# Performance work log

Hardware: AMD Instinct MI355X
Metric: run time of the kernel (lower is better)

## Reference

```python
import jax, jax.numpy as jnp
import numpy as np

D = 128        # embed_dims
P = 4          # num_points
G = 1          # num_groups
L = 4          # num_levels
NC = 6         # cameras
HB, WB = 200, 200
QN = HB * WB
NUM_LAYERS = 2
IMG_H, IMG_W = 256, 704
EPS = 1e-5
PC_MIN = np.array([-50.0, -50.0, -5.0], np.float32)
PC_EXT = np.array([100.0, 100.0, 8.0], np.float32)
LEVEL_HW = [(32, 88), (16, 44), (8, 22), (4, 11)]


def layer_norm(x, g, b):
    m = x.mean(-1, keepdims=True)
    v = jnp.mean((x - m) ** 2, axis=-1, keepdims=True)
    return (x - m) * jax.lax.rsqrt(v + 1e-5) * g + b


def bilinear(feat, u, v):
    # feat: (B,H,W,C); u,v: (B,N) normalized to [0,1]; zero padding, align_corners=False
    B, H, W, C = feat.shape
    x = u * W - 0.5
    y = v * H - 0.5
    x0f = jnp.floor(x)
    y0f = jnp.floor(y)
    wx = (x - x0f)[..., None]
    wy = (y - y0f)[..., None]
    x0 = x0f.astype(jnp.int32)
    y0 = y0f.astype(jnp.int32)
    bi = jnp.arange(B)[:, None]

    def gather(xi, yi):
        valid = ((xi >= 0) & (xi < W) & (yi >= 0) & (yi < H)).astype(feat.dtype)[..., None]
        return feat[bi, jnp.clip(yi, 0, H - 1), jnp.clip(xi, 0, W - 1)] * valid

    return (gather(x0, y0) * (1 - wx) * (1 - wy)
            + gather(x0 + 1, y0) * wx * (1 - wy)
            + gather(x0, y0 + 1) * (1 - wx) * wy
            + gather(x0 + 1, y0 + 1) * wx * wy)


def cam_contrib(l2i_n, hom, sw, cam_feats):
    # l2i_n: (B,4,4); hom: (B,Q,G,P,4); sw: (B,Q,G,P,L); cam_feats: L x (B,Hl,Wl,C)
    p2 = jnp.einsum('bij,bqgpj->bqgpi', l2i_n, hom)
    z = p2[..., 2]
    zc = jnp.maximum(z, EPS)
    u = p2[..., 0] / (zc * IMG_W)
    v = p2[..., 1] / (zc * IMG_H)
    mask = (z > EPS) & (u >= 0) & (u <= 1) & (v >= 0) & (v <= 1)
    B = hom.shape[0]
    uf = u.reshape(B, -1)
    vf = v.reshape(B, -1)
    out = jnp.zeros(hom.shape[:4] + (cam_feats[0].shape[-1],), cam_feats[0].dtype)
    for l in range(L):
        s = bilinear(cam_feats[l], uf, vf).reshape(B, -1, G, P, cam_feats[l].shape[-1])
        out = out + s * sw[..., l:l + 1]
    return out * mask[..., None].astype(out.dtype)


def forward(feat0, feat1, feat2, feat3, lidar2img, bev_query, bev_pos,
            pe_w1, pe_b1, pe_w2, pe_b2, conv1_w, conv1_b, conv2_w, conv2_b,
            off_w, off_b, sw_w, sw_b, cp_w1, cp_b1, cp_w2, cp_b2, cp_w3, cp_b3,
            ffn_w1, ffn_b1, ffn_w2, ffn_b2, n1_g, n1_b, n2_g, n2_b, n3_g, n3_b):
    # (b,n,C,h,w) -> (b,n,h,w,C), matching the decoder's rearrange (g=1)
    feats = [jnp.transpose(f, (0, 1, 3, 4, 2)) for f in (feat0, feat1, feat2, feat3)]
    B = bev_query.shape[0]
    pc_min = jnp.asarray(PC_MIN)
    pc_ext = jnp.asarray(PC_EXT)
    # position embedding of bev_pos is identical every layer
    pos_embed = jax.nn.relu(bev_pos @ pe_w1 + pe_b1) @ pe_w2 + pe_b2
    q = bev_query
    for _ in range(NUM_LAYERS):
        # in_conv: 1x1 conv + GELU + 5x5 conv on 200x200 BEV grid
        qe = (q + pos_embed).reshape(B, HB, WB, D)
        h = jax.nn.gelu(qe @ conv1_w + conv1_b, approximate=False)
        h = jax.lax.conv_general_dilated(h, conv2_w, (1, 1), 'SAME',
                                         dimension_numbers=('NHWC', 'HWIO', 'NHWC')) + conv2_b
        q = q + h.reshape(B, QN, D)
        q = layer_norm(q, n1_g, n1_b)
        # DetSegSampling
        off = (q @ off_w + off_b).reshape(B, QN, G, P, 3)
        ref = bev_pos[:, :, None, None, :] * pc_ext + pc_min
        pts = ref + off
        sw = jax.nn.softmax((q @ sw_w + sw_b).reshape(B, QN, G, P, L), axis=-1)
        hom = jnp.concatenate([pts, jnp.ones_like(pts[..., :1])], -1)
        acc = jnp.zeros((B, QN, G, P, D), q.dtype)
        for n in range(NC):
            acc = acc + cam_contrib(lidar2img[:, n], hom, sw,
                                    tuple(f[:, n] for f in feats))
        # 'b q g p c -> b q (p g c)' then 3-layer compressor MLP (1x1 convs)
        flat = jnp.transpose(acc, (0, 1, 3, 2, 4)).reshape(B, QN, P * G * D)
        h = jax.nn.relu(flat @ cp_w1 + cp_b1)
        h = jax.nn.relu(h @ cp_w2 + cp_b2)
        h = h @ cp_w3 + cp_b3
        q = q + h
        q = layer_norm(q, n2_g, n2_b)
        q = q + (jax.nn.relu(q @ ffn_w1 + ffn_b1) @ ffn_w2 + ffn_b2)
        q = layer_norm(q, n3_g, n3_b)
    return q


def _make_lidar2img():
    fx = fy = 500.0
    K = np.array([[fx, 0, IMG_W / 2, 0], [0, fy, IMG_H / 2, 0],
                  [0, 0, 1, 0], [0, 0, 0, 1]], np.float32)
    mats = []
    for n in range(NC):
        yaw = 2 * np.pi * n / NC
        c, s = np.cos(yaw), np.sin(yaw)
        # camera n looks along (cos yaw, sin yaw, 0), mounted 1.5m above lidar
        E = np.array([[s, -c, 0, 0], [0, 0, -1, 1.5], [c, s, 0, 0], [0, 0, 0, 1]], np.float32)
        mats.append(K @ E)
    return jnp.asarray(np.stack(mats))[None]  # (1,NC,4,4)


def setup_inputs() -> dict:
    key = jax.random.key(0)
    ks = jax.random.split(key, 24)
    sc = 0.02
    inp = {}
    for i, (h, w) in enumerate(LEVEL_HW):
        inp[f'feat{i}'] = jax.random.normal(ks[i], (1, NC, D, h, w), jnp.float32)
    inp['lidar2img'] = _make_lidar2img()
    inp['bev_query'] = jax.random.normal(ks[4], (1, QN, D), jnp.float32)
    inp['bev_pos'] = jax.random.uniform(ks[5], (1, QN, 3), jnp.float32)
    inp['pe_w1'] = jax.random.normal(ks[6], (3, 2 * D), jnp.float32) * sc
    inp['pe_b1'] = jnp.zeros((2 * D,), jnp.float32)
    inp['pe_w2'] = jax.random.normal(ks[7], (2 * D, D), jnp.float32) * sc
    inp['pe_b2'] = jnp.zeros((D,), jnp.float32)
    inp['conv1_w'] = jax.random.normal(ks[8], (D, D), jnp.float32) * sc
    inp['conv1_b'] = jnp.zeros((D,), jnp.float32)
    inp['conv2_w'] = jax.random.normal(ks[9], (5, 5, D, D), jnp.float32) * sc
    inp['conv2_b'] = jnp.zeros((D,), jnp.float32)
    inp['off_w'] = jax.random.normal(ks[10], (D, G * P * 3), jnp.float32) * 0.01
    inp['off_b'] = jax.random.uniform(ks[11], (G * P * 3,), jnp.float32, -0.5, 0.5)
    inp['sw_w'] = jax.random.normal(ks[12], (D, G * P * L), jnp.float32) * sc
    inp['sw_b'] = jnp.zeros((G * P * L,), jnp.float32)
    inp['cp_w1'] = jax.random.normal(ks[13], (P * G * D, 4 * D), jnp.float32) * sc
    inp['cp_b1'] = jnp.zeros((4 * D,), jnp.float32)
    inp['cp_w2'] = jax.random.normal(ks[14], (4 * D, 4 * D), jnp.float32) * sc
    inp['cp_b2'] = jnp.zeros((4 * D,), jnp.float32)
    inp['cp_w3'] = jax.random.normal(ks[15], (4 * D, D), jnp.float32) * sc
    inp['cp_b3'] = jnp.zeros((D,), jnp.float32)
    inp['ffn_w1'] = jax.random.normal(ks[16], (D, D), jnp.float32) * sc
    inp['ffn_b1'] = jnp.zeros((D,), jnp.float32)
    inp['ffn_w2'] = jax.random.normal(ks[17], (D, D), jnp.float32) * sc
    inp['ffn_b2'] = jnp.zeros((D,), jnp.float32)
    for i in (1, 2, 3):
        inp[f'n{i}_g'] = jnp.ones((D,), jnp.float32)
        inp[f'n{i}_b'] = jnp.zeros((D,), jnp.float32)
    return inp


def reference(feat0, feat1, feat2, feat3, lidar2img, bev_query, bev_pos,
              pe_w1, pe_b1, pe_w2, pe_b2, conv1_w, conv1_b, conv2_w, conv2_b,
              off_w, off_b, sw_w, sw_b, cp_w1, cp_b1, cp_w2, cp_b2, cp_w3, cp_b3,
              ffn_w1, ffn_b1, ffn_w2, ffn_b2, n1_g, n1_b, n2_g, n2_b, n3_g, n3_b):
    return forward(feat0, feat1, feat2, feat3, lidar2img, bev_query, bev_pos,
                   pe_w1, pe_b1, pe_w2, pe_b2, conv1_w, conv1_b, conv2_w, conv2_b,
                   off_w, off_b, sw_w, sw_b, cp_w1, cp_b1, cp_w2, cp_b2, cp_w3, cp_b3,
                   ffn_w1, ffn_b1, ffn_w2, ffn_b2, n1_g, n1_b, n2_g, n2_b, n3_g, n3_b)
```

## Files before the change

kernel.cpp:

```cpp
#include <hip/hip_runtime.h>
#include <hip/hip_bf16.h>

typedef unsigned short u16;
typedef unsigned char u8;
typedef __attribute__((ext_vector_type(8))) short bf16x8;
typedef __attribute__((ext_vector_type(4))) float f32x4;

#define DEV __device__ __forceinline__

DEV float b2f(u16 s){ return __uint_as_float(((unsigned)s) << 16); }
DEV u16 f2b(float f){
    unsigned u = __float_as_uint(f);
    u = u + 0x7fffu + ((u >> 16) & 1u);
    return (u16)(u >> 16);
}
DEV u8 f2f8(float v){
    int r = __builtin_amdgcn_cvt_pk_fp8_f32(v, v, 0, false);
    return (u8)(r & 0xff);
}
DEV unsigned f2f8x4(float a, float b, float c, float d){
    int lo = __builtin_amdgcn_cvt_pk_fp8_f32(a, b, 0, false);
    int r  = __builtin_amdgcn_cvt_pk_fp8_f32(c, d, lo, true);
    return (unsigned)r;
}
DEV void storeElem(float* p, float v){ *p = v; }
DEV void storeElem(u16* p, float v){ *p = f2b(v); }
DEV void storeElem(u8* p, float v){ *p = f2f8(v); }

template<int ACT> DEV float actf(float x){
    if (ACT == 1) return fmaxf(x, 0.f);
    if (ACT == 2) return 0.5f * x * (1.f + erff(x * 0.70710678118654752f));
    return x;
}

DEV void gload16(const void* g, void* l){
    __builtin_amdgcn_global_load_lds(
        (const __attribute__((address_space(1))) void*)g,
        (__attribute__((address_space(3))) void*)l, 16, 0, 0);
}

__global__ void transpose_feat(const float* __restrict__ in, u16* __restrict__ out,
                               int H, int W){
    int total = 6 * H * W * 32;
    int lin = blockIdx.x * 256 + threadIdx.x;
    if (lin >= total) return;
    int c4   = (lin & 31) * 4;
    int pix  = lin >> 5;
    int x    = pix % W;
    int rest = pix / W;
    int y    = rest % H;
    int n    = rest / H;
    int HW   = H * W;
    size_t ib = ((size_t)(n * 128 + c4) * H + y) * W + x;
    ushort4 v;
    v.x = f2b(in[ib]);
    v.y = f2b(in[ib + (size_t)HW]);
    v.z = f2b(in[ib + (size_t)2 * HW]);
    v.w = f2b(in[ib + (size_t)3 * HW]);
    *(ushort4*)&out[(size_t)pix * 128 + c4] = v;
}

__global__ void prep_wt(const float* __restrict__ w, u16* __restrict__ o, int K, int N){
    int id = blockIdx.x * 256 + threadIdx.x;
    if (id >= K * N) return;
    int n = id / K, k = id % K;
    o[id] = f2b(w[(size_t)k * N + n]);
}
__global__ void prep_wt_f8(const float* __restrict__ w, u8* __restrict__ o, int K, int N){
    int id = blockIdx.x * 256 + threadIdx.x;
    if (id >= K * N) return;
    int n = id / K, k = id % K;
    o[id] = f2f8(w[(size_t)k * N + n]);
}
__global__ void prep_osw_w(const float* __restrict__ off_w, const float* __restrict__ off_b,
                           const float* __restrict__ sw_w, const float* __restrict__ sw_b,
                           u16* __restrict__ owsT, float* __restrict__ obias){
    int id = blockIdx.x * 256 + threadIdx.x;
    if (id >= 4096) return;
    int n = id >> 7, k = id & 127;
    float w = (n < 12) ? off_w[k * 12 + n] : (n < 28) ? sw_w[k * 16 + (n - 12)] : 0.f;
    owsT[n * 128 + k] = f2b(w);
    if (k == 0) obias[n] = (n < 12) ? off_b[n] : (n < 28) ? sw_b[n - 12] : 0.f;
}
__global__ void prep_conv_w_f8(const float* __restrict__ w, u8* __restrict__ o){
    int id = blockIdx.x * 256 + threadIdx.x;
    if (id >= 51200) return;
    int slot = id & 15;
    int oc   = (id >> 4) & 127;
    int tap  = id >> 11;
    int ks = slot >> 2, kg = slot & 3;
    int ic0 = ks * 32 + kg * 8;
    u8 tmp[8];
#pragma unroll
    for (int j = 0; j < 8; j++)
        tmp[j] = f2f8(w[((size_t)tap * 128 + ic0 + j) * 128 + oc]);
    *(long*)&o[(size_t)tap * 16384 + ks * 4096 + kg * 1024 + oc * 8] = *(long*)tmp;
}
__global__ void prep_hid(const float* __restrict__ bev_pos,
                         const float* __restrict__ w1, const float* __restrict__ b1,
                         u16* __restrict__ hid){
    int id = blockIdx.x * 256 + threadIdx.x;
    if (id >= 2560000) return;
    int qi = id >> 6, c4 = (id & 63) * 4;
    float p0 = bev_pos[qi * 3 + 0];
    float p1 = bev_pos[qi * 3 + 1];
    float p2 = bev_pos[qi * 3 + 2];
    ushort4 v;
    u16* vp = (u16*)&v;
#pragma unroll
    for (int j = 0; j < 4; j++){
        int ch = c4 + j;
        float h = p0 * w1[ch] + p1 * w1[256 + ch] + p2 * w1[512 + ch] + b1[ch];
        vp[j] = f2b(fmaxf(h, 0.f));
    }
    *(ushort4*)&hid[(size_t)qi * 256 + c4] = v;
}

DEV void stage64(const u16* __restrict__ g, int ldk, u16* lds, int wv, int lane){
    const u16* gp = g + (size_t)(lane >> 3) * ldk + (lane & 7) * 8;
#pragma unroll
    for (int j = 0; j < 4; j++){
        int ch = wv + j * 4;
        gload16(gp + (size_t)ch * 8 * ldk, lds + ch * 512);
    }
}
DEV void stage64f8(const u8* __restrict__ g, int ldk, u8* lds, int wv, int lane){
    int rloc = lane >> 2;
#pragma unroll
    for (int j = 0; j < 2; j++){
        int ch = wv + j * 4;
        int row = ch * 16 + rloc;
        int sp  = (lane & 3) ^ ((row >> 1) & 3);
        gload16(g + (size_t)row * ldk + sp * 16, lds + ch * 1024);
    }
}

template<int K, int ACT, typename TOUT, int NBY = 0, int NBX = 0>
__global__ __launch_bounds__(256) void mfma_gemm(
    const u16* __restrict__ A, const u16* __restrict__ BT,
    const float* __restrict__ bias, TOUT* __restrict__ C, int Ntot){
    __shared__ u16 As[2][128 * 64];
    __shared__ u16 Bs[2][128 * 64];
    const int t = threadIdx.x, wv = t >> 6, lane = t & 63;
    int bx, by;
    if (NBY > 0){
        const int gpx = (NBX + 7) / 8;
        int xcd = blockIdx.x & 7, slot = blockIdx.x >> 3;
        bx = xcd * gpx + slot / NBY;
        by = slot % NBY;
        if (bx >= NBX) return;
    } else { bx = blockIdx.x; by = blockIdx.y; }
    const int r0 = bx * 128, n0 = by * 128;
    const int l15 = lane & 15, kg = lane >> 4;
    const int wr = (wv >> 1) * 64, wc = (wv & 1) * 64;
    f32x4 acc[4][4];
#pragma unroll
    for (int r = 0; r < 4; r++)
#pragma unroll
        for (int c = 0; c < 4; c++) acc[r][c] = (f32x4){0.f, 0.f, 0.f, 0.f};

    stage64(A + (size_t)r0 * K, K, As[0], wv, lane);
    stage64(BT + (size_t)n0 * K, K, Bs[0], wv, lane);
    __syncthreads();
    int buf = 0;
    for (int kc = 0; kc < K / 64; kc++){
        if (kc + 1 < K / 64){
            stage64(A + (size_t)r0 * K + (kc + 1) * 64, K, As[buf ^ 1], wv, lane);
            stage64(BT + (size_t)n0 * K + (kc + 1) * 64, K, Bs[buf ^ 1], wv, lane);
        }
#pragma unroll
        for (int ks = 0; ks < 2; ks++){
            bf16x8 af[4], bfr[4];
#pragma unroll
            for (int r = 0; r < 4; r++)
                af[r] = *(const bf16x8*)&As[buf][(wr + r * 16 + l15) * 64 + ks * 32 + kg * 8];
#pragma unroll
            for (int c = 0; c < 4; c++)
                bfr[c] = *(const bf16x8*)&Bs[buf][(wc + c * 16 + l15) * 64 + ks * 32 + kg * 8];
#pragma unroll
            for (int r = 0; r < 4; r++)
#pragma unroll
                for (int c = 0; c < 4; c++)
                    acc[r][c] = __builtin_amdgcn_mfma_f32_16x16x32_bf16(af[r], bfr[c], acc[r][c], 0, 0, 0);
        }
        __syncthreads();
        buf ^= 1;
    }
#pragma unroll
    for (int c = 0; c < 4; c++){
        int gcol = n0 + wc + c * 16 + l15;
        float bb = bias[gcol];
#pragma unroll
        for (int r = 0; r < 4; r++){
#pragma unroll
            for (int reg = 0; reg < 4; reg++){
                int grow = r0 + wr + r * 16 + kg * 4 + reg;
                storeElem(C + (size_t)grow * Ntot + gcol, actf<ACT>(acc[r][c][reg] + bb));
            }
        }
    }
}

template<int K, int ACT, typename TOUT, int NBY = 0, int NBX = 0>
__global__ __launch_bounds__(256) void mfma_gemm_f8(
    const u8* __restrict__ A, const u8* __restrict__ BT,
    const float* __restrict__ bias, TOUT* __restrict__ C, int Ntot){
    __shared__ __align__(16) u8 As[2][128 * 64];
    __shared__ __align__(16) u8 Bs[2][128 * 64];
    const int t = threadIdx.x, wv = t >> 6, lane = t & 63;
    int bx, by;
    if (NBY > 0){
        const int gpx = (NBX + 7) / 8;
        int xcd = blockIdx.x & 7, slot = blockIdx.x >> 3;
        bx = xcd * gpx + slot / NBY;
        by = slot % NBY;
        if (bx >= NBX) return;
    } else { bx = blockIdx.x; by = blockIdx.y; }
    const int r0 = bx * 128, n0 = by * 128;
    const int l15 = lane & 15, kg = lane >> 4;
    const int wr = (wv >> 1) * 64, wc = (wv & 1) * 64;
    f32x4 acc[4][4];
#pragma unroll
    for (int r = 0; r < 4; r++)
#pragma unroll
        for (int c = 0; c < 4; c++) acc[r][c] = (f32x4){0.f, 0.f, 0.f, 0.f};

    stage64f8(A + (size_t)r0 * K, K, As[0], wv, lane);
    stage64f8(BT + (size_t)n0 * K, K, Bs[0], wv, lane);
    __syncthreads();
    int buf = 0;
    for (int kc = 0; kc < K / 64; kc++){
        if (kc + 1 < K / 64){
            stage64f8(A + (size_t)r0 * K + (kc + 1) * 64, K, As[buf ^ 1], wv, lane);
            stage64f8(BT + (size_t)n0 * K + (kc + 1) * 64, K, Bs[buf ^ 1], wv, lane);
        }
#pragma unroll
        for (int ks = 0; ks < 2; ks++){
            long af[4], bfr[4];
#pragma unroll
            for (int r = 0; r < 4; r++){
                int row = wr + r * 16 + l15;
                int s8 = (ks * 4 + kg) ^ (row & 6);
                af[r] = *(const long*)&As[buf][row * 64 + s8 * 8];
            }
#pragma unroll
            for (int c = 0; c < 4; c++){
                int row = wc + c * 16 + l15;
                int s8 = (ks * 4 + kg) ^ (row & 6);
                bfr[c] = *(const long*)&Bs[buf][row * 64 + s8 * 8];
            }
#pragma unroll
            for (int r = 0; r < 4; r++)
#pragma unroll
                for (int c = 0; c < 4; c++)
                    acc[r][c] = __builtin_amdgcn_mfma_f32_16x16x32_fp8_fp8(af[r], bfr[c], acc[r][c], 0, 0, 0);
        }
        __syncthreads();
        buf ^= 1;
    }
#pragma unroll
    for (int c = 0; c < 4; c++){
        int gcol = n0 + wc + c * 16 + l15;
        float bb = bias[gcol];
#pragma unroll
        for (int r = 0; r < 4; r++){
#pragma unroll
            for (int reg = 0; reg < 4; reg++){
                int grow = r0 + wr + r * 16 + kg * 4 + reg;
                storeElem(C + (size_t)grow * Ntot + gcol, actf<ACT>(acc[r][c][reg] + bb));
            }
        }
    }
}

__global__ __launch_bounds__(256) void mfma_pos(
    const u16* __restrict__ A, const u16* __restrict__ BT,
    const float* __restrict__ bias, const float* __restrict__ bq,
    float* __restrict__ pos, u16* __restrict__ qp16){
    const int K = 256;
    __shared__ u16 As[2][128 * 64];
    __shared__ u16 Bs[2][128 * 64];
    const int t = threadIdx.x, wv = t >> 6, lane = t & 63;
    const int r0 = blockIdx.x * 128;
    const int l15 = lane & 15, kg = lane >> 4;
    const int wr = (wv >> 1) * 64, wc = (wv & 1) * 64;
    f32x4 acc[4][4];
#pragma unroll
    for (int r = 0; r < 4; r++)
#pragma unroll
        for (int c = 0; c < 4; c++) acc[r][c] = (f32x4){0.f, 0.f, 0.f, 0.f};

    stage64(A + (size_t)r0 * K, K, As[0], wv, lane);
    stage64(BT, K, Bs[0], wv, lane);
    __syncthreads();
    int buf = 0;
    for (int kc = 0; kc < 4; kc++){
        if (kc + 1 < 4){
            stage64(A + (size_t)r0 * K + (kc + 1) * 64, K, As[buf ^ 1], wv, lane);
            stage64(BT + (kc + 1) * 64, K, Bs[buf ^ 1], wv, lane);
        }
#pragma unroll
        for (int ks = 0; ks < 2; ks++){
            bf16x8 af[4], bfr[4];
#pragma unroll
            for (int r = 0; r < 4; r++)
                af[r] = *(const bf16x8*)&As[buf][(wr + r * 16 + l15) * 64 + ks * 32 + kg * 8];
#pragma unroll
            for (int c = 0; c < 4; c++)
                bfr[c] = *(const bf16x8*)&Bs[buf][(wc + c * 16 + l15) * 64 + ks * 32 + kg * 8];
#pragma unroll
            for (int r = 0; r < 4; r++)
#pragma unroll
                for (int c = 0; c < 4; c++)
                    acc[r][c] = __builtin_amdgcn_mfma_f32_16x16x32_bf16(af[r], bfr[c], acc[r][c], 0, 0, 0);
        }
        __syncthreads();
        buf ^= 1;
    }
#pragma unroll
    for (int c = 0; c < 4; c++){
        int gcol = wc + c * 16 + l15;
        float bb = bias[gcol];
#pragma unroll
        for (int r = 0; r < 4; r++){
#pragma unroll
            for (int reg = 0; reg < 4; reg++){
                int grow = r0 + wr + r * 16 + kg * 4 + reg;
                int growc = min(grow, 39999);
                float v = acc[r][c][reg] + bb;
                pos[(size_t)grow * 128 + gcol]  = v;
                qp16[(size_t)grow * 128 + gcol] = f2b(v + bq[(size_t)growc * 128 + gcol]);
            }
        }
    }
}

template<int K, int AUXM>
__global__ __launch_bounds__(256) void mfma_gemm_ln(
    const u16* __restrict__ A, const u16* __restrict__ BT,
    const float* __restrict__ bias, const float* __restrict__ qin,
    const float* __restrict__ gam, const float* __restrict__ bet,
    float* __restrict__ outf, u16* __restrict__ aux,
    const float* __restrict__ pos, int Mlim){
    __shared__ u16 As[2][128 * 64];
    __shared__ u16 Bs[2][128 * 64];
    const int t = threadIdx.x, wv = t >> 6, lane = t & 63;
    const int r0 = blockIdx.x * 128;
    const int l15 = lane & 15, kg = lane >> 4;
    const int wr = wv * 32;
    f32x4 acc[2][8];
#pragma unroll
    for (int r = 0; r < 2; r++)
#pragma unroll
        for (int c = 0; c < 8; c++) acc[r][c] = (f32x4){0.f, 0.f, 0.f, 0.f};

    stage64(A + (size_t)r0 * K, K, As[0], wv, lane);
    stage64(BT, K, Bs[0], wv, lane);
    __syncthreads();
    int buf = 0;
    for (int kc = 0; kc < K / 64; kc++){
        if (kc + 1 < K / 64){
            stage64(A + (size_t)r0 * K + (kc + 1) * 64, K, As[buf ^ 1], wv, lane);
            stage64(BT + (kc + 1) * 64, K, Bs[buf ^ 1], wv, lane);
        }
#pragma unroll
        for (int ks = 0; ks < 2; ks++){
            bf16x8 af[2], bfr[8];
#pragma unroll
            for (int r = 0; r < 2; r++)
                af[r] = *(const bf16x8*)&As[buf][(wr + r * 16 + l15) * 64 + ks * 32 + kg * 8];
#pragma unroll
            for (int c = 0; c < 8; c++)
                bfr[c] = *(const bf16x8*)&Bs[buf][(c * 16 + l15) * 64 + ks * 32 + kg * 8];
#pragma unroll
            for (int r = 0; r < 2; r++)
#pragma unroll
                for (int c = 0; c < 8; c++)
                    acc[r][c] = __builtin_amdgcn_mfma_f32_16x16x32_bf16(af[r], bfr[c], acc[r][c], 0, 0, 0);
        }
        __syncthreads();
        buf ^= 1;
    }
    float bb[8], gg[8], be[8];
#pragma unroll
    for (int c = 0; c < 8; c++){
        int col = c * 16 + l15;
        bb[c] = bias[col]; gg[c] = gam[col]; be[c] = bet[col];
    }
#pragma unroll
    for (int r = 0; r < 2; r++){
#pragma unroll
        for (int reg = 0; reg < 4; reg++){
            int grow = r0 + wr + r * 16 + kg * 4 + reg;
            const float* qrow = qin + (size_t)grow * 128;
            float s = 0.f, q2 = 0.f;
#pragma unroll
            for (int c = 0; c < 8; c++){
                float x = acc[r][c][reg] + bb[c] + qrow[c * 16 + l15];
                acc[r][c][reg] = x;
                s += x; q2 += x * x;
            }
#pragma unroll
            for (int m = 8; m >= 1; m >>= 1){
                s  += __shfl_xor(s, m, 64);
                q2 += __shfl_xor(q2, m, 64);
            }
            float mean = s * 0.0078125f;
            float var  = q2 * 0.0078125f - mean * mean;
            float rs   = rsqrtf(var + 1e-5f);
            bool wr_ok = grow < Mlim;
#pragma unroll
            for (int c = 0; c < 8; c++){
                float o = (acc[r][c][reg] - mean) * rs * gg[c] + be[c];
                int col = c * 16 + l15;
                if (wr_ok){
                    outf[(size_t)grow * 128 + col] = o;
                    if (AUXM == 1) aux[(size_t)grow * 128 + col] = f2b(o);
                    else if (AUXM == 2)
                        aux[(size_t)grow * 128 + col] = f2b(o + pos[(size_t)grow * 128 + col]);
                }
            }
        }
    }
}

template<int K, int AUXM>
__global__ __launch_bounds__(256) void mfma_gemm_ln_f8(
    const u8* __restrict__ A, const u8* __restrict__ BT,
    const float* __restrict__ bias, const float* __restrict__ qin,
    const float* __restrict__ gam, const float* __restrict__ bet,
    float* __restrict__ outf, u16* __restrict__ aux,
    const float* __restrict__ pos, int Mlim){
    __shared__ __align__(16) u8 As[2][128 * 64];
    __shared__ __align__(16) u8 Bs[2][128 * 64];
    const int t = threadIdx.x, wv = t >> 6, lane = t & 63;
    const int r0 = blockIdx.x * 128;
    const int l15 = lane & 15, kg = lane >> 4;
    const int wr = wv * 32;
    f32x4 acc[2][8];
#pragma unroll
    for (int r = 0; r < 2; r++)
#pragma unroll
        for (int c = 0; c < 8; c++) acc[r][c] = (f32x4){0.f, 0.f, 0.f, 0.f};

    stage64f8(A + (size_t)r0 * K, K, As[0], wv, lane);
    stage64f8(BT, K, Bs[0], wv, lane);
    __syncthreads();
    int buf = 0;
    for (int kc = 0; kc < K / 64; kc++){
        if (kc + 1 < K / 64){
            stage64f8(A + (size_t)r0 * K + (kc + 1) * 64, K, As[buf ^ 1], wv, lane);
            stage64f8(BT + (kc + 1) * 64, K, Bs[buf ^ 1], wv, lane);
        }
#pragma unroll
        for (int ks = 0; ks < 2; ks++){
            long af[2], bfr[8];
#pragma unroll
            for (int r = 0; r < 2; r++){
                int row = wr + r * 16 + l15;
                int s8 = (ks * 4 + kg) ^ (row & 6);
                af[r] = *(const long*)&As[buf][row * 64 + s8 * 8];
            }
#pragma unroll
            for (int c = 0; c < 8; c++){
                int row = c * 16 + l15;
                int s8 = (ks * 4 + kg) ^ (row & 6);
                bfr[c] = *(const long*)&Bs[buf][row * 64 + s8 * 8];
            }
#pragma unroll
            for (int r = 0; r < 2; r++)
#pragma unroll
                for (int c = 0; c < 8; c++)
                    acc[r][c] = __builtin_amdgcn_mfma_f32_16x16x32_fp8_fp8(af[r], bfr[c], acc[r][c], 0, 0, 0);
        }
        __syncthreads();
        buf ^= 1;
    }
    float bb[8], gg[8], be[8];
#pragma unroll
    for (int c = 0; c < 8; c++){
        int col = c * 16 + l15;
        bb[c] = bias[col]; gg[c] = gam[col]; be[c] = bet[col];
    }
#pragma unroll
    for (int r = 0; r < 2; r++){
#pragma unroll
        for (int reg = 0; reg < 4; reg++){
            int grow = r0 + wr + r * 16 + kg * 4 + reg;
            const float* qrow = qin + (size_t)grow * 128;
            float s = 0.f, q2 = 0.f;
#pragma unroll
            for (int c = 0; c < 8; c++){
                float x = acc[r][c][reg] + bb[c] + qrow[c * 16 + l15];
                acc[r][c][reg] = x;
                s += x; q2 += x * x;
            }
#pragma unroll
            for (int m = 8; m >= 1; m >>= 1){
                s  += __shfl_xor(s, m, 64);
                q2 += __shfl_xor(q2, m, 64);
            }
            float mean = s * 0.0078125f;
            float var  = q2 * 0.0078125f - mean * mean;
            float rs   = rsqrtf(var + 1e-5f);
            bool wr_ok = grow < Mlim;
#pragma unroll
            for (int c = 0; c < 8; c++){
                float o = (acc[r][c][reg] - mean) * rs * gg[c] + be[c];
                int col = c * 16 + l15;
                if (wr_ok){
                    outf[(size_t)grow * 128 + col] = o;
                    if (AUXM == 1) aux[(size_t)grow * 128 + col] = f2b(o);
                    else if (AUXM == 2)
                        aux[(size_t)grow * 128 + col] = f2b(o + pos[(size_t)grow * 128 + col]);
                }
            }
        }
    }
}

__global__ __launch_bounds__(256) void mfma_osw(
    const u16* __restrict__ A, const u16* __restrict__ BT,
    const float* __restrict__ bias, float* __restrict__ osw){
    __shared__ u16 As[2][128 * 64];
    __shared__ u16 Bs[2][32 * 64];
    const int t = threadIdx.x, wv = t >> 6, lane = t & 63;
    const int r0 = blockIdx.x * 128;
    const int l15 = lane & 15, kg = lane >> 4;
#pragma unroll
    for (int it = 0; it < 8; it++){
        int id = it * 256 + t;
        int row = id >> 4, slot = id & 15;
        uint4 v = *(const uint4*)&A[(size_t)(r0 + row) * 128 + slot * 8];
        *(uint4*)&As[slot >> 3][row * 64 + (slot & 7) * 8] = v;
    }
#pragma unroll
    for (int it = 0; it < 2; it++){
        int id = it * 256 + t;
        if (id < 512){
            int row = id >> 4, slot = id & 15;
            uint4 v = *(const uint4*)&BT[(size_t)row * 128 + slot * 8];
            *(uint4*)&Bs[slot >> 3][row * 64 + (slot & 7) * 8] = v;
        }
    }
    __syncthreads();
    f32x4 acc[2][2];
#pragma unroll
    for (int r = 0; r < 2; r++)
#pragma unroll
        for (int c = 0; c < 2; c++) acc[r][c] = (f32x4){0.f, 0.f, 0.f, 0.f};
#pragma unroll
    for (int ks = 0; ks < 4; ks++){
        int h = ks >> 1, koff = (ks & 1) * 32 + kg * 8;
        bf16x8 af[2], bfr[2];
#pragma unroll
        for (int r = 0; r < 2; r++)
            af[r] = *(const bf16x8*)&As[h][(wv * 32 + r * 16 + l15) * 64 + koff];
#pragma unroll
        for (int c = 0; c < 2; c++)
            bfr[c] = *(const bf16x8*)&Bs[h][(c * 16 + l15) * 64 + koff];
#pragma unroll
        for (int r = 0; r < 2; r++)
#pragma unroll
            for (int c = 0; c < 2; c++)
                acc[r][c] = __builtin_amdgcn_mfma_f32_16x16x32_bf16(af[r], bfr[c], acc[r][c], 0, 0, 0);
    }
#pragma unroll
    for (int c = 0; c < 2; c++){
        int gcol = c * 16 + l15;
        float bb = bias[gcol];
#pragma unroll
        for (int r = 0; r < 2; r++)
#pragma unroll
            for (int reg = 0; reg < 4; reg++){
                int grow = r0 + wv * 32 + r * 16 + kg * 4 + reg;
                osw[(size_t)grow * 32 + gcol] = acc[r][c][reg] + bb;
            }
    }
}

__global__ __launch_bounds__(256) void proj_kernel(
    const float* __restrict__ osw, const float* __restrict__ bev_pos,
    const float* __restrict__ l2i, float* __restrict__ ent, int* __restrict__ cntb){
    int id = blockIdx.x * 256 + threadIdx.x;
    int qi = id >> 2, p = id & 3;
    const float* row = osw + (size_t)qi * 32;
    float px = bev_pos[qi * 3 + 0] * 100.f - 50.f + row[p * 3 + 0];
    float py = bev_pos[qi * 3 + 1] * 100.f - 50.f + row[p * 3 + 1];
    float pz = bev_pos[qi * 3 + 2] * 8.f   - 5.f  + row[p * 3 + 2];
    float lg[4];
#pragma unroll
    for (int l = 0; l < 4; l++) lg[l] = row[12 + p * 4 + l];
    float mx = fmaxf(fmaxf(lg[0], lg[1]), fmaxf(lg[2], lg[3]));
    float den = 0.f, sw[4];
#pragma unroll
    for (int l = 0; l < 4; l++){ sw[l] = expf(lg[l] - mx); den += sw[l]; }
    float inv = 1.f / den;
#pragma unroll
    for (int l = 0; l < 4; l++) sw[l] *= inv;

    const int HS[4] = {32, 16, 8, 4};
    const int WS[4] = {88, 44, 22, 11};
    const unsigned LOFF[4] = {0u, 2162688u, 2703360u, 2838528u};
    int cnt = 0;
    for (int cam = 0; cam < 6; cam++){
        const float* M = l2i + cam * 16;
        float t0 = M[0] * px + M[1] * py + M[2]  * pz + M[3];
        float t1 = M[4] * px + M[5] * py + M[6]  * pz + M[7];
        float z  = M[8] * px + M[9] * py + M[10] * pz + M[11];
        float zc = fmaxf(z, 1e-5f);
        float u = t0 / (zc * 704.f);
        float v = t1 / (zc * 256.f);
        if (!((z > 1e-5f) && u >= 0.f && u <= 1.f && v >= 0.f && v <= 1.f)) continue;
#pragma unroll
        for (int l = 0; l < 4; l++){
            const int Hl = HS[l], Wl = WS[l];
            float xx = u * (float)Wl - 0.5f;
            float yy = v * (float)Hl - 0.5f;
            float xf = floorf(xx), yf = floorf(yy);
            float wx = xx - xf, wy = yy - yf;
            int ix = (int)xf, iy = (int)yf;
            float sl = sw[l];
            float wx0 = (ix >= 0)      ? 1.f - wx : 0.f;
            float wx1 = (ix < Wl - 1)  ? wx       : 0.f;
            float wy0 = (iy >= 0)      ? 1.f - wy : 0.f;
            float wy1 = (iy < Hl - 1)  ? wy       : 0.f;
            int x0c = max(ix, 0), x1c = min(ix + 1, Wl - 1);
            int y0c = max(iy, 0), y1c = min(iy + 1, Hl - 1);
            unsigned base = LOFF[l] + (unsigned)cam * (unsigned)(Hl * Wl * 128)
                          + (unsigned)(y0c * Wl + x0c) * 128u;
            unsigned dxdy = (unsigned)((x1c - x0c) * 128)
                          | ((unsigned)((y1c - y0c) * Wl * 128) << 16);
            if (cnt < 8){
                float* ep = ent + ((size_t)cnt * 160000 + id) * 8;
                float4 w4;
                w4.x = sl * wx0 * wy0; w4.y = sl * wx1 * wy0;
                w4.z = sl * wx0 * wy1; w4.w = sl * wx1 * wy1;
                *(float4*)ep = w4;
                float4 m4;
                m4.x = __uint_as_float(base); m4.y = __uint_as_float(dxdy);
                m4.z = 0.f; m4.w = 0.f;
                *(float4*)(ep + 4) = m4;
                cnt++;
            }
        }
    }
    cntb[id] = cnt;
}

DEV void fma8(float* acc, uint4 v, float w){
    acc[0] = fmaf(__uint_as_float(v.x << 16), w, acc[0]);
    acc[1] = fmaf(__uint_as_float(v.x & 0xffff0000u), w, acc[1]);
    acc[2] = fmaf(__uint_as_float(v.y << 16), w, acc[2]);
    acc[3] = fmaf(__uint_as_float(v.y & 0xffff0000u), w, acc[3]);
    acc[4] = fmaf(__uint_as_float(v.z << 16), w, acc[4]);
    acc[5] = fmaf(__uint_as_float(v.z & 0xffff0000u), w, acc[5]);
    acc[6] = fmaf(__uint_as_float(v.w << 16), w, acc[6]);
    acc[7] = fmaf(__uint_as_float(v.w & 0xffff0000u), w, acc[7]);
}

__global__ __launch_bounds__(256) void sample_kernel(
    const float* __restrict__ ent, const int* __restrict__ cntb,
    const u16* __restrict__ ftbase, u8* __restrict__ flat){
    const int t = threadIdx.x;
    const int lane = t & 15;
    const int id = blockIdx.x * 16 + (t >> 4);
    const int d0 = lane * 8;
    const int cnt = cntb[id];
    float acc[8] = {0, 0, 0, 0, 0, 0, 0, 0};

    float4 wA, wB; float2 mA, mB;
    if (cnt > 0){
        const float* ep = ent + ((size_t)id) * 8;
        wA = *(const float4*)ep;
        mA = *(const float2*)(ep + 4);
    }
    for (int e = 0; e < cnt; e++){
        if (e + 1 < cnt){
            const float* ep = ent + ((size_t)(e + 1) * 160000 + id) * 8;
            wB = *(const float4*)ep;
            mB = *(const float2*)(ep + 4);
        }
        unsigned base = __float_as_uint(mA.x) + (unsigned)d0;
        unsigned dxdy = __float_as_uint(mA.y);
        unsigned dx = dxdy & 0xffffu, dy = dxdy >> 16;
        uint4 v00 = *(const uint4*)(ftbase + base);
        uint4 v10 = *(const uint4*)(ftbase + base + dx);
        uint4 v01 = *(const uint4*)(ftbase + base + dy);
        uint4 v11 = *(const uint4*)(ftbase + base + dx + dy);
        fma8(acc, v00, wA.x);
        fma8(acc, v10, wA.y);
        fma8(acc, v01, wA.z);
        fma8(acc, v11, wA.w);
        wA = wB; mA = mB;
    }
    uint2 o;
    o.x = f2f8x4(acc[0], acc[1], acc[2], acc[3]);
    o.y = f2f8x4(acc[4], acc[5], acc[6], acc[7]);
    *(uint2*)&flat[(size_t)id * 128 + d0] = o;
}

#define ALOAD(S, DST) if ((S) < 100){                                                 \
    const int tap_ = (S) >> 2, ks_ = (S) & 3;                                         \
    const int ky_ = tap_ / 5, kx_ = tap_ - ky_ * 5;                                   \
    const int s8_ = ks_ * 4 + kg;                                                     \
    _Pragma("unroll")                                                                 \
    for (int fb = 0; fb < 2; fb++){                                                   \
        _Pragma("unroll")                                                             \
        for (int fp = 0; fp < 2; fp++){                                               \
            int pr_ = fb * 4 + (l15 >> 2) + ky_;                                      \
            int pc_ = fp * 4 + (l15 & 3) + kx_;                                       \
            int pix_ = pr_ * 12 + pc_;                                                \
            int sw_ = ((s8_ >> 1) ^ (pc_ + 4 * pr_)) & 7;                             \
            DST[fb * 2 + fp] = *(const long*)((const char*)Ps + pix_ * 128            \
                                              + sw_ * 16 + (s8_ & 1) * 8);            \
        }                                                                             \
    }                                                                                 \
}
#define CMFMA(CURA, CURB) {                                                           \
    _Pragma("unroll")                                                                 \
    for (int fr = 0; fr < 4; fr++){                                                   \
        acc[fr][0] = __builtin_amdgcn_mfma_f32_16x16x32_fp8_fp8(CURA[fr], CURB[0], acc[fr][0], 0, 0, 0); \
        acc[fr][1] = __builtin_amdgcn_mfma_f32_16x16x32_fp8_fp8(CURA[fr], CURB[1], acc[fr][1], 0, 0, 0); \
    }                                                                                 \
}
#define LOADB(S, DST) if ((S) < 100){                                                 \
    const u8* wp_ = wfrag + ((S) >> 2) * 16384 + ((S) & 3) * 4096                     \
                   + kg * 1024 + (wc + l15) * 8;                                      \
    DST[0] = *(const long*)(wp_);                                                     \
    DST[1] = *(const long*)(wp_ + 128);                                               \
}

__global__ __launch_bounds__(256, 4) void conv5_ln(
    const u8* __restrict__ in,
    const u8* __restrict__ wfrag,
    const float* __restrict__ bias,
    const float* __restrict__ qin,
    const float* __restrict__ gam, const float* __restrict__ bet,
    float* __restrict__ qb, u16* __restrict__ q16){
    __shared__ __align__(16) u8 Ps[144 * 128];
    const int t = threadIdx.x, wv = t >> 6, lane = t & 63;
    const int bx = blockIdx.x % 25, by = blockIdx.x / 25;
    const int x0 = bx * 8, y0 = by * 8;
    const int l15 = lane & 15, kg = lane >> 4;
    const int wc = wv * 32;

#pragma unroll
    for (int it = 0; it < 5; it++){
        int id = it * 256 + t;
        if (id < 1152){
            int pix = id >> 3, slot = id & 7;
            int pr = pix / 12, pc = pix - pr * 12;
            int gy = y0 + pr - 2, gx = x0 + pc - 2;
            uint4 v = {0u, 0u, 0u, 0u};
            if (gy >= 0 && gy < 200 && gx >= 0 && gx < 200)
                v = *(const uint4*)&in[(size_t)(gy * 200 + gx) * 128 + slot * 16];
            int s = (slot ^ (pc + 4 * pr)) & 7;
            *(uint4*)((char*)Ps + pix * 128 + s * 16) = v;
        }
    }
    f32x4 acc[4][2];
#pragma unroll
    for (int r = 0; r < 4; r++){
        acc[r][0] = (f32x4){0.f, 0.f, 0.f, 0.f};
        acc[r][1] = (f32x4){0.f, 0.f, 0.f, 0.f};
    }

    long b0[2], b1[2], b2[2], b3[2];
    LOADB(0, b0); LOADB(1, b1); LOADB(2, b2);
    __syncthreads();

    long aA[4], aB[4];
    ALOAD(0, aA);

    for (int i = 0; i < 25; i++){
        int s = i * 4;
        LOADB(s + 3, b3); ALOAD(s + 1, aB); CMFMA(aA, b0);
        LOADB(s + 4, b0); ALOAD(s + 2, aA); CMFMA(aB, b1);
        LOADB(s + 5, b1); ALOAD(s + 3, aB); CMFMA(aA, b2);
        LOADB(s + 6, b2); ALOAD(s + 4, aA); CMFMA(aB, b3);
    }
    __syncthreads();

    float* part = (float*)Ps;
    float bb[2], gg[2], be[2];
#pragma unroll
    for (int c = 0; c < 2; c++){
        int oc = wc + c * 16 + l15;
        bb[c] = bias[oc]; gg[c] = gam[oc]; be[c] = bet[oc];
    }
#pragma unroll
    for (int fb = 0; fb < 2; fb++){
#pragma unroll
        for (int fp = 0; fp < 2; fp++){
#pragma unroll
            for (int reg = 0; reg < 4; reg++){
                int py = fb * 4 + kg, px = fp * 4 + reg;
                int lp = py * 8 + px;
                int grow = (y0 + py) * 200 + x0 + px;
                const float* qrow = qin + (size_t)grow * 128;
                float s = 0.f, q2 = 0.f;
#pragma unroll
                for (int c = 0; c < 2; c++){
                    float x = acc[fb * 2 + fp][c][reg] + bb[c] + qrow[wc + c * 16 + l15];
                    acc[fb * 2 + fp][c][reg] = x;
                    s += x; q2 += x * x;
                }
#pragma unroll
                for (int msk = 8; msk >= 1; msk >>= 1){
                    s  += __shfl_xor(s, msk, 64);
                    q2 += __shfl_xor(q2, msk, 64);
                }
                if (l15 == 0){
                    part[lp * 8 + wv * 2 + 0] = s;
                    part[lp * 8 + wv * 2 + 1] = q2;
                }
            }
        }
    }
    __syncthreads();
#pragma unroll
    for (int fb = 0; fb < 2; fb++){
#pragma unroll
        for (int fp = 0; fp < 2; fp++){
#pragma unroll
            for (int reg = 0; reg < 4; reg++){
                int py = fb * 4 + kg, px = fp * 4 + reg;
                int lp = py * 8 + px;
                int grow = (y0 + py) * 200 + x0 + px;
                float s  = part[lp * 8 + 0] + part[lp * 8 + 2] + part[lp * 8 + 4] + part[lp * 8 + 6];
                float q2 = part[lp * 8 + 1] + part[lp * 8 + 3] + part[lp * 8 + 5] + part[lp * 8 + 7];
                float mean = s * 0.0078125f;
                float var  = q2 * 0.0078125f - mean * mean;
                float rs   = rsqrtf(var + 1e-5f);
#pragma unroll
                for (int c = 0; c < 2; c++){
                    int oc = wc + c * 16 + l15;
                    float o = (acc[fb * 2 + fp][c][reg] - mean) * rs * gg[c] + be[c];
                    qb[(size_t)grow * 128 + oc]  = o;
                    q16[(size_t)grow * 128 + oc] = f2b(o);
                }
            }
        }
    }
}

extern "C" void kernel_launch(void* const* d_in, const int* in_sizes, int n_in,
                              void* d_out, int out_size, void* d_ws, size_t ws_size,
                              hipStream_t stream){
    const float* feat0   = (const float*)d_in[0];
    const float* feat1   = (const float*)d_in[1];
    const float* feat2   = (const float*)d_in[2];
    const float* feat3   = (const float*)d_in[3];
    const float* l2i     = (const float*)d_in[4];
    const float* bev_q   = (const float*)d_in[5];
    const float* bev_pos = (const float*)d_in[6];
    const float* pe_w1   = (const float*)d_in[7];
    const float* pe_b1   = (const float*)d_in[8];
    const float* pe_w2   = (const float*)d_in[9];
    const float* pe_b2   = (const float*)d_in[10];
    const float* conv1_w = (const float*)d_in[11];
    const float* conv1_b = (const float*)d_in[12];
    const float* conv2_w = (const float*)d_in[13];
    const float* conv2_b = (const float*)d_in[14];
    const float* off_w   = (const float*)d_in[15];
    const float* off_b   = (const float*)d_in[16];
    const float* sw_w    = (const float*)d_in[17];
    const float* sw_b    = (const float*)d_in[18];
    const float* cp_w1   = (const float*)d_in[19];
    const float* cp_b1   = (const float*)d_in[20];
    const float* cp_w2   = (const float*)d_in[21];
    const float* cp_b2   = (const float*)d_in[22];
    const float* cp_w3   = (const float*)d_in[23];
    const float* cp_b3   = (const float*)d_in[24];
    const float* ffn_w1  = (const float*)d_in[25];
    const float* ffn_b1  = (const float*)d_in[26];
    const float* ffn_w2  = (const float*)d_in[27];
    const float* ffn_b2  = (const float*)d_in[28];
    const float* n1g = (const float*)d_in[29];
    const float* n1b = (const float*)d_in[30];
    const float* n2g = (const float*)d_in[31];
    const float* n2b = (const float*)d_in[32];
    const float* n3g = (const float*)d_in[33];
    const float* n3b = (const float*)d_in[34];

    float* base   = (float*)d_ws;
    float* pos    = base;
    float* qb     = base + 5128192;
    float* hbuf   = base + 10256384;
    u8*    h18    = (u8*)hbuf;
    float* ent    = hbuf;
    u16*   q16    = (u16*)(base + 20512768);
    u16*   qpos16 = (u16*)(base + 23076864);
    int*   cntb   = (int*)qpos16;
    u8*    bufA8  = (u8*)(base + 25640960);
    float* osw    = (float*)(base + 25640960 + 1310720);
    u16*   bufA16 = (u16*)(base + 25640960);
    u8*    flat8  = (u8*)(base + 28205056);
    u16*   hid16  = (u16*)flat8;
    u16*   ft0    = (u16*)(base + 38461440);
    u16*   ft1    = ft0 + 6 * 32 * 88 * 128;
    u16*   ft2    = ft1 + 6 * 16 * 44 * 128;
    u16*   ft3    = ft2 + 6 * 8 * 22 * 128;
    u8*    w1t8   = (u8*)(base + 39897600);
    u8*    w2t8   = w1t8 + 512 * 512;
    u8*    w3t8   = w2t8 + 512 * 512;
    u16*   wc1t   = (u16*)(base + 40192512);
    u16*   wf1t   = (u16*)(base + 40200704);
    u16*   wf2t   = (u16*)(base + 40208896);
    u16*   owsT   = (u16*)(base + 40217088);
    float* obias  = (float*)(base + 40219136);
    u8*    wcs8   = (u8*)(base + 40219168);
    u16*   pw2t   = (u16*)(base + 40424168);
    float* outp   = (float*)d_out;

    transpose_feat<<<(6 * 32 * 88 * 32 + 255) / 256, 256, 0, stream>>>(feat0, ft0, 32, 88);
    transpose_feat<<<(6 * 16 * 44 * 32 + 255) / 256, 256, 0, stream>>>(feat1, ft1, 16, 44);
    transpose_feat<<<(6 * 8 * 22 * 32 + 255) / 256, 256, 0, stream>>>(feat2, ft2, 8, 22);
    transpose_feat<<<(6 * 4 * 11 * 32 + 255) / 256, 256, 0, stream>>>(feat3, ft3, 4, 11);
    prep_wt_f8<<<(512 * 512 + 255) / 256, 256, 0, stream>>>(cp_w1, w1t8, 512, 512);
    prep_wt_f8<<<(512 * 512 + 255) / 256, 256, 0, stream>>>(cp_w2, w2t8, 512, 512);
    prep_wt_f8<<<(512 * 128 + 255) / 256, 256, 0, stream>>>(cp_w3, w3t8, 512, 128);
    prep_wt<<<(128 * 128 + 255) / 256, 256, 0, stream>>>(conv1_w, wc1t, 128, 128);
    prep_wt<<<(128 * 128 + 255) / 256, 256, 0, stream>>>(ffn_w1, wf1t, 128, 128);
    prep_wt<<<(128 * 128 + 255) / 256, 256, 0, stream>>>(ffn_w2, wf2t, 128, 128);
    prep_wt<<<(256 * 128 + 255) / 256, 256, 0, stream>>>(pe_w2, pw2t, 256, 128);
    prep_osw_w<<<16, 256, 0, stream>>>(off_w, off_b, sw_w, sw_b, owsT, obias);
    prep_conv_w_f8<<<(51200 + 255) / 256, 256, 0, stream>>>(conv2_w, wcs8);
    prep_hid<<<10000, 256, 0, stream>>>(bev_pos, pe_w1, pe_b1, hid16);
    mfma_pos<<<313, 256, 0, stream>>>(hid16, pw2t, pe_b2, bev_q, pos, qpos16);

    for (int layer = 0; layer < 2; layer++){
        const float* qin = layer ? qb : bev_q;
        mfma_gemm<128, 2, u8><<<dim3(313, 1), 256, 0, stream>>>(qpos16, wc1t, conv1_b, bufA8, 128);
        conv5_ln<<<625, 256, 0, stream>>>(bufA8, wcs8, conv2_b, qin, n1g, n1b, qb, q16);
        mfma_osw<<<313, 256, 0, stream>>>(q16, owsT, obias, osw);
        proj_kernel<<<625, 256, 0, stream>>>(osw, bev_pos, l2i, ent, cntb);
        sample_kernel<<<10000, 256, 0, stream>>>(ent, cntb, ft0, flat8);
        mfma_gemm_f8<512, 1, u8, 4, 313><<<1280, 256, 0, stream>>>(flat8, w1t8, cp_b1, h18, 512);
        mfma_gemm_f8<512, 1, u8, 4, 313><<<1280, 256, 0, stream>>>(h18, w2t8, cp_b2, flat8, 512);
        mfma_gemm_ln_f8<512, 1><<<313, 256, 0, stream>>>(flat8, w3t8, cp_b3, qb, n2g, n2b,
                                                         qb, q16, nullptr, 40064);
        mfma_gemm<128, 1, u16><<<dim3(313, 1), 256, 0, stream>>>(q16, wf1t, ffn_b1, bufA16, 128);
        if (layer == 0)
            mfma_gemm_ln<128, 2><<<313, 256, 0, stream>>>(bufA16, wf2t, ffn_b2, qb, n3g, n3b,
                                                          qb, qpos16, pos, 40064);
        else
            mfma_gemm_ln<128, 0><<<313, 256, 0, stream>>>(bufA16, wf2t, ffn_b2, qb, n3g, n3b,
                                                          outp, nullptr, nullptr, 40000);
    }
}
```

Baseline: 446.9 us.

## Fuse FFN GEMMs into one kernel and store camera features as FP8

```diff
diff --git a/kernel.cpp b/kernel.cpp
--- a/kernel.cpp
+++ b/kernel.cpp
@@ -5,6 +5,7 @@
 typedef unsigned char u8;
 typedef __attribute__((ext_vector_type(8))) short bf16x8;
 typedef __attribute__((ext_vector_type(4))) float f32x4;
+typedef __attribute__((ext_vector_type(2))) float f32x2;
 
 #define DEV __device__ __forceinline__
 
@@ -39,7 +40,7 @@
         (__attribute__((address_space(3))) void*)l, 16, 0, 0);
 }
 
-__global__ void transpose_feat(const float* __restrict__ in, u16* __restrict__ out,
+__global__ void transpose_feat(const float* __restrict__ in, u8* __restrict__ out,
                                int H, int W){
     int total = 6 * H * W * 32;
     int lin = blockIdx.x * 256 + threadIdx.x;
@@ -52,12 +53,9 @@
     int n    = rest / H;
     int HW   = H * W;
     size_t ib = ((size_t)(n * 128 + c4) * H + y) * W + x;
-    ushort4 v;
-    v.x = f2b(in[ib]);
-    v.y = f2b(in[ib + (size_t)HW]);
-    v.z = f2b(in[ib + (size_t)2 * HW]);
-    v.w = f2b(in[ib + (size_t)3 * HW]);
-    *(ushort4*)&out[(size_t)pix * 128 + c4] = v;
+    unsigned v4 = f2f8x4(in[ib], in[ib + (size_t)HW],
+                         in[ib + (size_t)2 * HW], in[ib + (size_t)3 * HW]);
+    *(unsigned*)&out[(size_t)pix * 128 + c4] = v4;
 }
 
 __global__ void prep_wt(const float* __restrict__ w, u16* __restrict__ o, int K, int N){
@@ -335,10 +333,11 @@
     }
 }
 
-template<int K, int AUXM>
-__global__ __launch_bounds__(256) void mfma_gemm_ln(
-    const u16* __restrict__ A, const u16* __restrict__ BT,
-    const float* __restrict__ bias, const float* __restrict__ qin,
+template<int AUXM>
+__global__ __launch_bounds__(256) void mfma_ffn_ln(
+    const u16* __restrict__ A, const u16* __restrict__ W1T,
+    const float* __restrict__ b1, const u16* __restrict__ W2T,
+    const float* __restrict__ b2, const float* __restrict__ qin,
     const float* __restrict__ gam, const float* __restrict__ bet,
     float* __restrict__ outf, u16* __restrict__ aux,
     const float* __restrict__ pos, int Mlim){
@@ -354,38 +353,72 @@
 #pragma unroll
         for (int c = 0; c < 8; c++) acc[r][c] = (f32x4){0.f, 0.f, 0.f, 0.f};
 
-    stage64(A + (size_t)r0 * K, K, As[0], wv, lane);
-    stage64(BT, K, Bs[0], wv, lane);
-    __syncthreads();
-    int buf = 0;
-    for (int kc = 0; kc < K / 64; kc++){
-        if (kc + 1 < K / 64){
-            stage64(A + (size_t)r0 * K + (kc + 1) * 64, K, As[buf ^ 1], wv, lane);
-            stage64(BT + (kc + 1) * 64, K, Bs[buf ^ 1], wv, lane);
-        }
+    stage64(A + (size_t)r0 * 128, 128, As[0], wv, lane);
+    stage64(A + (size_t)r0 * 128 + 64, 128, As[1], wv, lane);
+    stage64(W1T, 128, Bs[0], wv, lane);
+    stage64(W1T + 64, 128, Bs[1], wv, lane);
+    __syncthreads();
+#pragma unroll
+    for (int kc = 0; kc < 2; kc++){
 #pragma unroll
         for (int ks = 0; ks < 2; ks++){
             bf16x8 af[2], bfr[8];
 #pragma unroll
             for (int r = 0; r < 2; r++)
-                af[r] = *(const bf16x8*)&As[buf][(wr + r * 16 + l15) * 64 + ks * 32 + kg * 8];
+                af[r] = *(const bf16x8*)&As[kc][(wr + r * 16 + l15) * 64 + ks * 32 + kg * 8];
 #pragma unroll
             for (int c = 0; c < 8; c++)
-                bfr[c] = *(const bf16x8*)&Bs[buf][(c * 16 + l15) * 64 + ks * 32 + kg * 8];
+                bfr[c] = *(const bf16x8*)&Bs[kc][(c * 16 + l15) * 64 + ks * 32 + kg * 8];
 #pragma unroll
             for (int r = 0; r < 2; r++)
 #pragma unroll
                 for (int c = 0; c < 8; c++)
                     acc[r][c] = __builtin_amdgcn_mfma_f32_16x16x32_bf16(af[r], bfr[c], acc[r][c], 0, 0, 0);
         }
-        __syncthreads();
-        buf ^= 1;
-    }
-    float bb[8], gg[8], be[8];
+    }
+    __syncthreads();
+    stage64(W2T, 128, Bs[0], wv, lane);
+    stage64(W2T + 64, 128, Bs[1], wv, lane);
 #pragma unroll
     for (int c = 0; c < 8; c++){
         int col = c * 16 + l15;
-        bb[c] = bias[col]; gg[c] = gam[col]; be[c] = bet[col];
+        float bb1 = b1[col];
+#pragma unroll
+        for (int r = 0; r < 2; r++)
+#pragma unroll
+            for (int reg = 0; reg < 4; reg++){
+                int rowl = wr + r * 16 + kg * 4 + reg;
+                As[col >> 6][rowl * 64 + (col & 63)] = f2b(fmaxf(acc[r][c][reg] + bb1, 0.f));
+            }
+    }
+    __syncthreads();
+#pragma unroll
+    for (int r = 0; r < 2; r++)
+#pragma unroll
+        for (int c = 0; c < 8; c++) acc[r][c] = (f32x4){0.f, 0.f, 0.f, 0.f};
+#pragma unroll
+    for (int kc = 0; kc < 2; kc++){
+#pragma unroll
+        for (int ks = 0; ks < 2; ks++){
+            bf16x8 af[2], bfr[8];
+#pragma unroll
+            for (int r = 0; r < 2; r++)
+                af[r] = *(const bf16x8*)&As[kc][(wr + r * 16 + l15) * 64 + ks * 32 + kg * 8];
+#pragma unroll
+            for (int c = 0; c < 8; c++)
+                bfr[c] = *(const bf16x8*)&Bs[kc][(c * 16 + l15) * 64 + ks * 32 + kg * 8];
+#pragma unroll
+            for (int r = 0; r < 2; r++)
+#pragma unroll
+                for (int c = 0; c < 8; c++)
+                    acc[r][c] = __builtin_amdgcn_mfma_f32_16x16x32_bf16(af[r], bfr[c], acc[r][c], 0, 0, 0);
+        }
+    }
+    float bb[8], gg[8], be[8];
+#pragma unroll
+    for (int c = 0; c < 8; c++){
+        int col = c * 16 + l15;
+        bb[c] = b2[col]; gg[c] = gam[col]; be[c] = bet[col];
     }
 #pragma unroll
     for (int r = 0; r < 2; r++){
@@ -415,8 +448,7 @@
                 int col = c * 16 + l15;
                 if (wr_ok){
                     outf[(size_t)grow * 128 + col] = o;
-                    if (AUXM == 1) aux[(size_t)grow * 128 + col] = f2b(o);
-                    else if (AUXM == 2)
+                    if (AUXM == 2)
                         aux[(size_t)grow * 128 + col] = f2b(o + pos[(size_t)grow * 128 + col]);
                 }
             }
@@ -648,20 +680,24 @@
     cntb[id] = cnt;
 }
 
-DEV void fma8(float* acc, uint4 v, float w){
-    acc[0] = fmaf(__uint_as_float(v.x << 16), w, acc[0]);
-    acc[1] = fmaf(__uint_as_float(v.x & 0xffff0000u), w, acc[1]);
-    acc[2] = fmaf(__uint_as_float(v.y << 16), w, acc[2]);
-    acc[3] = fmaf(__uint_as_float(v.y & 0xffff0000u), w, acc[3]);
-    acc[4] = fmaf(__uint_as_float(v.z << 16), w, acc[4]);
-    acc[5] = fmaf(__uint_as_float(v.z & 0xffff0000u), w, acc[5]);
-    acc[6] = fmaf(__uint_as_float(v.w << 16), w, acc[6]);
-    acc[7] = fmaf(__uint_as_float(v.w & 0xffff0000u), w, acc[7]);
+DEV void fma8f8(float* acc, uint2 v, float w){
+    f32x2 p0 = __builtin_amdgcn_cvt_pk_f32_fp8(v.x, false);
+    f32x2 p1 = __builtin_amdgcn_cvt_pk_f32_fp8(v.x, true);
+    f32x2 p2 = __builtin_amdgcn_cvt_pk_f32_fp8(v.y, false);
+    f32x2 p3 = __builtin_amdgcn_cvt_pk_f32_fp8(v.y, true);
+    acc[0] = fmaf(p0.x, w, acc[0]);
+    acc[1] = fmaf(p0.y, w, acc[1]);
+    acc[2] = fmaf(p1.x, w, acc[2]);
+    acc[3] = fmaf(p1.y, w, acc[3]);
+    acc[4] = fmaf(p2.x, w, acc[4]);
+    acc[5] = fmaf(p2.y, w, acc[5]);
+    acc[6] = fmaf(p3.x, w, acc[6]);
+    acc[7] = fmaf(p3.y, w, acc[7]);
 }
 
 __global__ __launch_bounds__(256) void sample_kernel(
     const float* __restrict__ ent, const int* __restrict__ cntb,
-    const u16* __restrict__ ftbase, u8* __restrict__ flat){
+    const u8* __restrict__ ftbase, u8* __restrict__ flat){
     const int t = threadIdx.x;
     const int lane = t & 15;
     const int id = blockIdx.x * 16 + (t >> 4);
@@ -684,14 +720,14 @@
         unsigned base = __float_as_uint(mA.x) + (unsigned)d0;
         unsigned dxdy = __float_as_uint(mA.y);
         unsigned dx = dxdy & 0xffffu, dy = dxdy >> 16;
-        uint4 v00 = *(const uint4*)(ftbase + base);
-        uint4 v10 = *(const uint4*)(ftbase + base + dx);
-        uint4 v01 = *(const uint4*)(ftbase + base + dy);
-        uint4 v11 = *(const uint4*)(ftbase + base + dx + dy);
-        fma8(acc, v00, wA.x);
-        fma8(acc, v10, wA.y);
-        fma8(acc, v01, wA.z);
-        fma8(acc, v11, wA.w);
+        uint2 v00 = *(const uint2*)(ftbase + base);
+        uint2 v10 = *(const uint2*)(ftbase + base + dx);
+        uint2 v01 = *(const uint2*)(ftbase + base + dy);
+        uint2 v11 = *(const uint2*)(ftbase + base + dx + dy);
+        fma8f8(acc, v00, wA.x);
+        fma8f8(acc, v10, wA.y);
+        fma8f8(acc, v01, wA.z);
+        fma8f8(acc, v11, wA.w);
         wA = wB; mA = mB;
     }
     uint2 o;
@@ -895,13 +931,12 @@
     int*   cntb   = (int*)qpos16;
     u8*    bufA8  = (u8*)(base + 25640960);
     float* osw    = (float*)(base + 25640960 + 1310720);
-    u16*   bufA16 = (u16*)(base + 25640960);
     u8*    flat8  = (u8*)(base + 28205056);
     u16*   hid16  = (u16*)flat8;
-    u16*   ft0    = (u16*)(base + 38461440);
-    u16*   ft1    = ft0 + 6 * 32 * 88 * 128;
-    u16*   ft2    = ft1 + 6 * 16 * 44 * 128;
-    u16*   ft3    = ft2 + 6 * 8 * 22 * 128;
+    u8*    ft0    = (u8*)(base + 38461440);
+    u8*    ft1    = ft0 + 6 * 32 * 88 * 128;
+    u8*    ft2    = ft1 + 6 * 16 * 44 * 128;
+    u8*    ft3    = ft2 + 6 * 8 * 22 * 128;
     u8*    w1t8   = (u8*)(base + 39897600);
     u8*    w2t8   = w1t8 + 512 * 512;
     u8*    w3t8   = w2t8 + 512 * 512;
@@ -941,12 +976,11 @@
         mfma_gemm_f8<512, 1, u8, 4, 313><<<1280, 256, 0, stream>>>(h18, w2t8, cp_b2, flat8, 512);
         mfma_gemm_ln_f8<512, 1><<<313, 256, 0, stream>>>(flat8, w3t8, cp_b3, qb, n2g, n2b,
                                                          qb, q16, nullptr, 40064);
-        mfma_gemm<128, 1, u16><<<dim3(313, 1), 256, 0, stream>>>(q16, wf1t, ffn_b1, bufA16, 128);
         if (layer == 0)
-            mfma_gemm_ln<128, 2><<<313, 256, 0, stream>>>(bufA16, wf2t, ffn_b2, qb, n3g, n3b,
-                                                          qb, qpos16, pos, 40064);
+            mfma_ffn_ln<2><<<313, 256, 0, stream>>>(q16, wf1t, ffn_b1, wf2t, ffn_b2,
+                                                    qb, n3g, n3b, qb, qpos16, pos, 40064);
         else
-            mfma_gemm_ln<128, 0><<<313, 256, 0, stream>>>(bufA16, wf2t, ffn_b2, qb, n3g, n3b,
-                                                          outp, nullptr, nullptr, 40000);
-    }
-}
+            mfma_ffn_ln<0><<<313, 256, 0, stream>>>(q16, wf1t, ffn_b1, wf2t, ffn_b2,
+                                                    qb, n3g, n3b, outp, nullptr, nullptr, 40000);
+    }
+}
```

Result: faster. 436.6 us (-2.3%).
